# Kernel tuning notes

Hardware: AMD Instinct MI355X
Metric: run time of the kernel (lower is better)

## Reference

```python
import jax, jax.numpy as jnp
import numpy as np

T, G, K, N = 8192, 8, 1024, 2048

def setup_inputs() -> dict:
    key = jax.random.key(0)
    k1, k2, k3 = jax.random.split(key, 3)
    x = jax.random.normal(k1, (T, K), dtype=jnp.float32)
    w = jax.random.normal(k2, (G, N, K), dtype=jnp.float32) * 0.02
    # cumulative end-offsets per group: sorted, last entry == T (covers all tokens)
    offs = jnp.sort(jax.random.randint(k3, (G,), 0, T).astype(jnp.int32))
    offs = offs.at[-1].set(T)
    return {"input": x, "weight": w, "grouped_mm_offs": offs}

def reference(input, weight, grouped_mm_offs):
    # grouped_mm(input, weight.transpose(1,2), offs): token t in group g iff
    # offs[g-1] <= t < offs[g]; out[t] = input[t] @ weight[g].T
    t = input.shape[0]
    g = weight.shape[0]
    gid = jnp.searchsorted(grouped_mm_offs, jnp.arange(t), side="right")  # [T]
    out = jnp.zeros((t, weight.shape[1]), dtype=input.dtype)
    for gi in range(g):  # fixed small expert loop; data dims stay vectorized
        xg = jnp.where((gid == gi)[:, None], input, jnp.zeros((), input.dtype))
        out = out + xg @ weight[gi].T
    return out
```

## Files before the change

### kernel.cpp

```cpp
#include <hip/hip_runtime.h>
#include <hip/hip_bf16.h>


#define T_DIM 8192
#define G_DIM 8
#define K_DIM 1024
#define N_DIM 2048
#define MAX_PAIRS 72

using short8  = __attribute__((ext_vector_type(8))) short;
using f32x4   = __attribute__((ext_vector_type(4))) float;
using ushort8 = __attribute__((ext_vector_type(8))) unsigned short;

typedef __attribute__((address_space(1))) void gvoid;
typedef __attribute__((address_space(3))) void lvoid;

__global__ __launch_bounds__(256) void cvt_kernel(const float* __restrict__ x,
                                                  const float* __restrict__ w,
                                                  ushort8* __restrict__ xb,
                                                  ushort8* __restrict__ wb,
                                                  int n8x, int n8tot) {
  const int stride = gridDim.x * blockDim.x;
  for (int i = blockIdx.x * blockDim.x + threadIdx.x; i < n8tot; i += 2 * stride) {
#pragma unroll
    for (int u = 0; u < 2; ++u) {
      const int idx = i + u * stride;
      if (idx >= n8tot) break;
      const f32x4* s; ushort8* d; int j;
      if (idx < n8x) { s = (const f32x4*)x; d = xb; j = idx; }
      else           { s = (const f32x4*)w; d = wb; j = idx - n8x; }
      f32x4 v0 = __builtin_nontemporal_load(&s[2 * j]);
      f32x4 v1 = __builtin_nontemporal_load(&s[2 * j + 1]);
      ushort8 o;
      o[0] = __builtin_bit_cast(unsigned short, __float2bfloat16(v0[0]));
      o[1] = __builtin_bit_cast(unsigned short, __float2bfloat16(v0[1]));
      o[2] = __builtin_bit_cast(unsigned short, __float2bfloat16(v0[2]));
      o[3] = __builtin_bit_cast(unsigned short, __float2bfloat16(v0[3]));
      o[4] = __builtin_bit_cast(unsigned short, __float2bfloat16(v1[0]));
      o[5] = __builtin_bit_cast(unsigned short, __float2bfloat16(v1[1]));
      o[6] = __builtin_bit_cast(unsigned short, __float2bfloat16(v1[2]));
      o[7] = __builtin_bit_cast(unsigned short, __float2bfloat16(v1[3]));
      d[j] = o;
    }
  }
}

__global__ __launch_bounds__(256, 4) void grouped_gemm_kernel(
    const __hip_bfloat16* __restrict__ xb,
    const __hip_bfloat16* __restrict__ wb,
    const int* __restrict__ offs,
    float* __restrict__ out) {
  int offv[G_DIM];
#pragma unroll
  for (int i = 0; i < G_DIM; ++i) offv[i] = offs[i];

  const int p = blockIdx.y;
  int g = -1, tile = 0, lo = 0, hi = 0, pre = 0;
#pragma unroll
  for (int gi = 0; gi < G_DIM; ++gi) {
    const int l = gi ? offv[gi - 1] : 0;
    const int h = offv[gi];
    const int t0 = l >> 7;
    const int cnt = (h > l) ? (((h + 127) >> 7) - t0) : 0;
    if (g < 0 && p < pre + cnt) { g = gi; tile = t0 + (p - pre); lo = l; hi = h; }
    pre += cnt;
  }
  if (g < 0) return;

  const int m0 = tile * 128;
  const int n0 = blockIdx.x * 128;

  __shared__ __align__(16) __hip_bfloat16 As[128 * 64];
  __shared__ __align__(16) __hip_bfloat16 Bs[128 * 64];

  const __hip_bfloat16* wg = wb + (size_t)g * N_DIM * K_DIM;

  const int lane = threadIdx.x & 63;
  const int wid  = threadIdx.x >> 6;
  const int wm   = wid >> 1;
  const int wn   = wid & 1;

  const int srow = lane >> 3;
  const int scol = ((lane & 7) ^ srow) * 8;

  f32x4 acc[4][4] = {};

  for (int kk = 0; kk < K_DIM / 64; ++kk) {
    const int k0 = kk * 64;
#pragma unroll
    for (int i = 0; i < 4; ++i) {
      const int j   = wid * 4 + i;
      const int row = j * 8 + srow;
      const __hip_bfloat16* ga = xb + (size_t)(m0 + row) * K_DIM + k0 + scol;
      const __hip_bfloat16* gb = wg + (size_t)(n0 + row) * K_DIM + k0 + scol;
      __builtin_amdgcn_global_load_lds((gvoid*)ga, (lvoid*)(As + j * 512), 16, 0, 0);
      __builtin_amdgcn_global_load_lds((gvoid*)gb, (lvoid*)(Bs + j * 512), 16, 0, 0);
    }
    __syncthreads();

#pragma unroll
    for (int ks = 0; ks < 2; ++ks) {
      const int kb  = ks * 4 + (lane >> 4);
      const int off = ((kb ^ (lane & 7)) * 8);
      short8 a[4], b[4];
#pragma unroll
      for (int mt = 0; mt < 4; ++mt)
        a[mt] = *reinterpret_cast<const short8*>(
            As + (wm * 64 + mt * 16 + (lane & 15)) * 64 + off);
#pragma unroll
      for (int nt = 0; nt < 4; ++nt)
        b[nt] = *reinterpret_cast<const short8*>(
            Bs + (wn * 64 + nt * 16 + (lane & 15)) * 64 + off);
#pragma unroll
      for (int mt = 0; mt < 4; ++mt)
#pragma unroll
        for (int nt = 0; nt < 4; ++nt)
          acc[mt][nt] = __builtin_amdgcn_mfma_f32_16x16x32_bf16(
              a[mt], b[nt], acc[mt][nt], 0, 0, 0);
    }
    __syncthreads();
  }

  const int quad = lane >> 4;
#pragma unroll
  for (int mt = 0; mt < 4; ++mt) {
    const int rbase = m0 + wm * 64 + mt * 16 + quad * 4;
#pragma unroll
    for (int r = 0; r < 4; ++r) {
      const int row = rbase + r;
      if (row < lo || row >= hi) continue;
#pragma unroll
      for (int nt = 0; nt < 4; ++nt) {
        const int col = n0 + wn * 64 + nt * 16 + (lane & 15);
        out[(size_t)row * N_DIM + col] = acc[mt][nt][r];
      }
    }
  }
}

__global__ __launch_bounds__(256) void fallback_kernel(
    const float* __restrict__ x, const float* __restrict__ w,
    const int* __restrict__ offs, float* __restrict__ out) {
  __shared__ float xs[K_DIM];
  const int t = blockIdx.y;
  int g = 0;
  while (g < G_DIM - 1 && offs[g] <= t) ++g;
  for (int i = threadIdx.x; i < K_DIM; i += blockDim.x)
    xs[i] = x[(size_t)t * K_DIM + i];
  __syncthreads();
  const int n = blockIdx.x * blockDim.x + threadIdx.x;
  const float* wr = w + ((size_t)g * N_DIM + n) * K_DIM;
  float s = 0.f;
  for (int k = 0; k < K_DIM; ++k) s += xs[k] * wr[k];
  out[(size_t)t * N_DIM + n] = s;
}

extern "C" void kernel_launch(void* const* d_in, const int* in_sizes, int n_in,
                              void* d_out, int out_size, void* d_ws, size_t ws_size,
                              hipStream_t stream) {
  const float* x    = (const float*)d_in[0];
  const float* w    = (const float*)d_in[1];
  const int*   offs = (const int*)d_in[2];
  float*       out  = (float*)d_out;

  const size_t x_elems = (size_t)T_DIM * K_DIM;
  const size_t w_elems = (size_t)G_DIM * N_DIM * K_DIM;
  const size_t need    = (x_elems + w_elems) * sizeof(__hip_bfloat16);

  if (ws_size < need) {
    fallback_kernel<<<dim3(N_DIM / 256, T_DIM), 256, 0, stream>>>(x, w, offs, out);
    return;
  }

  __hip_bfloat16* xb = (__hip_bfloat16*)d_ws;
  __hip_bfloat16* wb = xb + x_elems;

  const int n8x   = (int)(x_elems / 8);
  const int n8tot = (int)((x_elems + w_elems) / 8);
  cvt_kernel<<<4096, 256, 0, stream>>>(x, w, (ushort8*)xb, (ushort8*)wb,
                                       n8x, n8tot);

  grouped_gemm_kernel<<<dim3(N_DIM / 128, MAX_PAIRS), 256, 0, stream>>>(
      xb, wb, offs, out);
}
```

Baseline: 183.9 us.

## Triple-buffer LDS loads, widen tile to 128x256 with 512 threads, remap blocks

```diff
diff --git a/kernel.cpp b/kernel.cpp
--- a/kernel.cpp
+++ b/kernel.cpp
@@ -7,6 +7,8 @@
 #define K_DIM 1024
 #define N_DIM 2048
 #define MAX_PAIRS 72
+#define PPX (MAX_PAIRS / 8)
+#define NT (K_DIM / 64)
 
 using short8  = __attribute__((ext_vector_type(8))) short;
 using f32x4   = __attribute__((ext_vector_type(4))) float;
@@ -45,16 +47,20 @@
   }
 }
 
-__global__ __launch_bounds__(256, 4) void grouped_gemm_kernel(
+__global__ __launch_bounds__(512) void grouped_gemm_kernel(
     const __hip_bfloat16* __restrict__ xb,
     const __hip_bfloat16* __restrict__ wb,
     const int* __restrict__ offs,
     float* __restrict__ out) {
+  const int v  = blockIdx.y * 8 + blockIdx.x;
+  const int p  = (v & 7) * PPX + ((v >> 3) % PPX);
+  const int nb = (v >> 3) / PPX;
+  const int n0 = nb * 256;
+
   int offv[G_DIM];
 #pragma unroll
   for (int i = 0; i < G_DIM; ++i) offv[i] = offs[i];
 
-  const int p = blockIdx.y;
   int g = -1, tile = 0, lo = 0, hi = 0, pre = 0;
 #pragma unroll
   for (int gi = 0; gi < G_DIM; ++gi) {
@@ -68,58 +74,94 @@
   if (g < 0) return;
 
   const int m0 = tile * 128;
-  const int n0 = blockIdx.x * 128;
-
-  __shared__ __align__(16) __hip_bfloat16 As[128 * 64];
-  __shared__ __align__(16) __hip_bfloat16 Bs[128 * 64];
+
+  __shared__ __align__(16) __hip_bfloat16 As[3 * 128 * 64];
+  __shared__ __align__(16) __hip_bfloat16 Bs[3 * 256 * 64];
 
   const __hip_bfloat16* wg = wb + (size_t)g * N_DIM * K_DIM;
 
   const int lane = threadIdx.x & 63;
   const int wid  = threadIdx.x >> 6;
-  const int wm   = wid >> 1;
-  const int wn   = wid & 1;
+  const int wm   = wid >> 2;
+  const int wn   = wid & 3;
 
   const int srow = lane >> 3;
   const int scol = ((lane & 7) ^ srow) * 8;
 
+  const __hip_bfloat16* gA0 = xb + (size_t)(m0 + (wid * 2 + 0) * 8 + srow) * K_DIM + scol;
+  const __hip_bfloat16* gA1 = xb + (size_t)(m0 + (wid * 2 + 1) * 8 + srow) * K_DIM + scol;
+  const __hip_bfloat16* gB0 = wg + (size_t)(n0 + (wid * 4 + 0) * 8 + srow) * K_DIM + scol;
+  const __hip_bfloat16* gB1 = wg + (size_t)(n0 + (wid * 4 + 1) * 8 + srow) * K_DIM + scol;
+  const __hip_bfloat16* gB2 = wg + (size_t)(n0 + (wid * 4 + 2) * 8 + srow) * K_DIM + scol;
+  const __hip_bfloat16* gB3 = wg + (size_t)(n0 + (wid * 4 + 3) * 8 + srow) * K_DIM + scol;
+
+  __hip_bfloat16* Ad = As + (wid * 2) * 512 + lane * 8;
+  __hip_bfloat16* Bd = Bs + (wid * 4) * 512 + lane * 8;
+
+  auto stage = [&](int tt, int bb) {
+    const int ko = tt * 64;
+    __hip_bfloat16* Adb = Ad + bb * (128 * 64);
+    __hip_bfloat16* Bdb = Bd + bb * (256 * 64);
+    __builtin_amdgcn_global_load_lds((gvoid*)(gA0 + ko), (lvoid*)(Adb),        16, 0, 0);
+    __builtin_amdgcn_global_load_lds((gvoid*)(gA1 + ko), (lvoid*)(Adb + 512),  16, 0, 0);
+    __builtin_amdgcn_global_load_lds((gvoid*)(gB0 + ko), (lvoid*)(Bdb),        16, 0, 0);
+    __builtin_amdgcn_global_load_lds((gvoid*)(gB1 + ko), (lvoid*)(Bdb + 512),  16, 0, 0);
+    __builtin_amdgcn_global_load_lds((gvoid*)(gB2 + ko), (lvoid*)(Bdb + 1024), 16, 0, 0);
+    __builtin_amdgcn_global_load_lds((gvoid*)(gB3 + ko), (lvoid*)(Bdb + 1536), 16, 0, 0);
+  };
+
   f32x4 acc[4][4] = {};
 
-  for (int kk = 0; kk < K_DIM / 64; ++kk) {
-    const int k0 = kk * 64;
-#pragma unroll
-    for (int i = 0; i < 4; ++i) {
-      const int j   = wid * 4 + i;
-      const int row = j * 8 + srow;
-      const __hip_bfloat16* ga = xb + (size_t)(m0 + row) * K_DIM + k0 + scol;
-      const __hip_bfloat16* gb = wg + (size_t)(n0 + row) * K_DIM + k0 + scol;
-      __builtin_amdgcn_global_load_lds((gvoid*)ga, (lvoid*)(As + j * 512), 16, 0, 0);
-      __builtin_amdgcn_global_load_lds((gvoid*)gb, (lvoid*)(Bs + j * 512), 16, 0, 0);
-    }
-    __syncthreads();
-
+  auto compute_tile = [&](int bb) {
+    const __hip_bfloat16* Ab = As + bb * (128 * 64);
+    const __hip_bfloat16* Bb = Bs + bb * (256 * 64);
+    short8 a[2][4], b[2][4];
 #pragma unroll
     for (int ks = 0; ks < 2; ++ks) {
       const int kb  = ks * 4 + (lane >> 4);
-      const int off = ((kb ^ (lane & 7)) * 8);
-      short8 a[4], b[4];
+      const int off = (kb ^ (lane & 7)) * 8;
 #pragma unroll
       for (int mt = 0; mt < 4; ++mt)
-        a[mt] = *reinterpret_cast<const short8*>(
-            As + (wm * 64 + mt * 16 + (lane & 15)) * 64 + off);
+        a[ks][mt] = *reinterpret_cast<const short8*>(
+            Ab + (wm * 64 + mt * 16 + (lane & 15)) * 64 + off);
 #pragma unroll
       for (int nt = 0; nt < 4; ++nt)
-        b[nt] = *reinterpret_cast<const short8*>(
-            Bs + (wn * 64 + nt * 16 + (lane & 15)) * 64 + off);
+        b[ks][nt] = *reinterpret_cast<const short8*>(
+            Bb + (wn * 64 + nt * 16 + (lane & 15)) * 64 + off);
+    }
+    __builtin_amdgcn_s_setprio(1);
+#pragma unroll
+    for (int ks = 0; ks < 2; ++ks)
 #pragma unroll
       for (int mt = 0; mt < 4; ++mt)
 #pragma unroll
         for (int nt = 0; nt < 4; ++nt)
           acc[mt][nt] = __builtin_amdgcn_mfma_f32_16x16x32_bf16(
-              a[mt], b[nt], acc[mt][nt], 0, 0, 0);
-    }
-    __syncthreads();
-  }
+              a[ks][mt], b[ks][nt], acc[mt][nt], 0, 0, 0);
+    __builtin_amdgcn_s_setprio(0);
+  };
+
+  stage(0, 0);
+  stage(1, 1);
+
+  for (int t = 0; t < NT - 2; ++t) {
+    const int buf = t % 3;
+    stage(t + 2, (t + 2) % 3);
+    asm volatile("s_waitcnt vmcnt(12)" ::: "memory");
+    __builtin_amdgcn_s_barrier();
+    asm volatile("" ::: "memory");
+    compute_tile(buf);
+    asm volatile("" ::: "memory");
+    __builtin_amdgcn_s_barrier();
+  }
+  asm volatile("s_waitcnt vmcnt(6)" ::: "memory");
+  __builtin_amdgcn_s_barrier();
+  asm volatile("" ::: "memory");
+  compute_tile((NT - 2) % 3);
+  asm volatile("s_waitcnt vmcnt(0)" ::: "memory");
+  __builtin_amdgcn_s_barrier();
+  asm volatile("" ::: "memory");
+  compute_tile((NT - 1) % 3);
 
   const int quad = lane >> 4;
 #pragma unroll
@@ -180,6 +222,6 @@
   cvt_kernel<<<4096, 256, 0, stream>>>(x, w, (ushort8*)xb, (ushort8*)wb,
                                        n8x, n8tot);
 
-  grouped_gemm_kernel<<<dim3(N_DIM / 128, MAX_PAIRS), 256, 0, stream>>>(
+  grouped_gemm_kernel<<<dim3(N_DIM / 256, MAX_PAIRS), 512, 0, stream>>>(
       xb, wb, offs, out);
 }
```

New measurement: 206.1 us. 1.12x slower.

## Fuse weight fp32-to-bf16 conversion into GEMM with register-prefetched B tiles

Applied to the files above, without the earlier changes.

```diff
diff --git a/kernel.cpp b/kernel.cpp
--- a/kernel.cpp
+++ b/kernel.cpp
@@ -7,6 +7,7 @@
 #define K_DIM 1024
 #define N_DIM 2048
 #define MAX_PAIRS 72
+#define NT (K_DIM / 64)
 
 using short8  = __attribute__((ext_vector_type(8))) short;
 using f32x4   = __attribute__((ext_vector_type(4))) float;
@@ -15,65 +16,58 @@
 typedef __attribute__((address_space(1))) void gvoid;
 typedef __attribute__((address_space(3))) void lvoid;
 
-__global__ __launch_bounds__(256) void cvt_kernel(const float* __restrict__ x,
-                                                  const float* __restrict__ w,
-                                                  ushort8* __restrict__ xb,
-                                                  ushort8* __restrict__ wb,
-                                                  int n8x, int n8tot) {
+__global__ __launch_bounds__(256) void cvt_x_kernel(const float* __restrict__ x,
+                                                    ushort8* __restrict__ xb,
+                                                    int n8) {
   const int stride = gridDim.x * blockDim.x;
-  for (int i = blockIdx.x * blockDim.x + threadIdx.x; i < n8tot; i += 2 * stride) {
-#pragma unroll
-    for (int u = 0; u < 2; ++u) {
-      const int idx = i + u * stride;
-      if (idx >= n8tot) break;
-      const f32x4* s; ushort8* d; int j;
-      if (idx < n8x) { s = (const f32x4*)x; d = xb; j = idx; }
-      else           { s = (const f32x4*)w; d = wb; j = idx - n8x; }
-      f32x4 v0 = __builtin_nontemporal_load(&s[2 * j]);
-      f32x4 v1 = __builtin_nontemporal_load(&s[2 * j + 1]);
-      ushort8 o;
-      o[0] = __builtin_bit_cast(unsigned short, __float2bfloat16(v0[0]));
-      o[1] = __builtin_bit_cast(unsigned short, __float2bfloat16(v0[1]));
-      o[2] = __builtin_bit_cast(unsigned short, __float2bfloat16(v0[2]));
-      o[3] = __builtin_bit_cast(unsigned short, __float2bfloat16(v0[3]));
-      o[4] = __builtin_bit_cast(unsigned short, __float2bfloat16(v1[0]));
-      o[5] = __builtin_bit_cast(unsigned short, __float2bfloat16(v1[1]));
-      o[6] = __builtin_bit_cast(unsigned short, __float2bfloat16(v1[2]));
-      o[7] = __builtin_bit_cast(unsigned short, __float2bfloat16(v1[3]));
-      d[j] = o;
-    }
+  for (int i = blockIdx.x * blockDim.x + threadIdx.x; i < n8; i += stride) {
+    f32x4 v0 = __builtin_nontemporal_load(&((const f32x4*)x)[2 * i]);
+    f32x4 v1 = __builtin_nontemporal_load(&((const f32x4*)x)[2 * i + 1]);
+    ushort8 o;
+    o[0] = __builtin_bit_cast(unsigned short, __float2bfloat16(v0[0]));
+    o[1] = __builtin_bit_cast(unsigned short, __float2bfloat16(v0[1]));
+    o[2] = __builtin_bit_cast(unsigned short, __float2bfloat16(v0[2]));
+    o[3] = __builtin_bit_cast(unsigned short, __float2bfloat16(v0[3]));
+    o[4] = __builtin_bit_cast(unsigned short, __float2bfloat16(v1[0]));
+    o[5] = __builtin_bit_cast(unsigned short, __float2bfloat16(v1[1]));
+    o[6] = __builtin_bit_cast(unsigned short, __float2bfloat16(v1[2]));
+    o[7] = __builtin_bit_cast(unsigned short, __float2bfloat16(v1[3]));
+    xb[i] = o;
   }
 }
 
 __global__ __launch_bounds__(256, 4) void grouped_gemm_kernel(
     const __hip_bfloat16* __restrict__ xb,
-    const __hip_bfloat16* __restrict__ wb,
+    const float* __restrict__ w,
     const int* __restrict__ offs,
     float* __restrict__ out) {
+  const int v  = blockIdx.y * 16 + blockIdx.x;
+  const int c  = v & 7;
+  const int l  = v >> 3;
+  const int nb = c * 2 + (l & 1);
+  const int p  = l >> 1;
+  const int n0 = nb * 128;
+
   int offv[G_DIM];
 #pragma unroll
   for (int i = 0; i < G_DIM; ++i) offv[i] = offs[i];
 
-  const int p = blockIdx.y;
   int g = -1, tile = 0, lo = 0, hi = 0, pre = 0;
 #pragma unroll
   for (int gi = 0; gi < G_DIM; ++gi) {
-    const int l = gi ? offv[gi - 1] : 0;
-    const int h = offv[gi];
-    const int t0 = l >> 7;
-    const int cnt = (h > l) ? (((h + 127) >> 7) - t0) : 0;
-    if (g < 0 && p < pre + cnt) { g = gi; tile = t0 + (p - pre); lo = l; hi = h; }
+    const int lb = gi ? offv[gi - 1] : 0;
+    const int hb = offv[gi];
+    const int t0 = lb >> 7;
+    const int cnt = (hb > lb) ? (((hb + 127) >> 7) - t0) : 0;
+    if (g < 0 && p < pre + cnt) { g = gi; tile = t0 + (p - pre); lo = lb; hi = hb; }
     pre += cnt;
   }
   if (g < 0) return;
 
   const int m0 = tile * 128;
-  const int n0 = blockIdx.x * 128;
 
   __shared__ __align__(16) __hip_bfloat16 As[128 * 64];
   __shared__ __align__(16) __hip_bfloat16 Bs[128 * 64];
-
-  const __hip_bfloat16* wg = wb + (size_t)g * N_DIM * K_DIM;
 
   const int lane = threadIdx.x & 63;
   const int wid  = threadIdx.x >> 6;
@@ -82,21 +76,62 @@
 
   const int srow = lane >> 3;
   const int scol = ((lane & 7) ^ srow) * 8;
+  const int lcol = (lane & 7) * 8;
+
+  const __hip_bfloat16* gA[4];
+  const float*          gB[4];
+  __hip_bfloat16*       Bd[4];
+#pragma unroll
+  for (int i = 0; i < 4; ++i) {
+    const int j   = wid * 4 + i;
+    const int row = j * 8 + srow;
+    gA[i] = xb + (size_t)(m0 + row) * K_DIM + scol;
+    gB[i] = w + ((size_t)g * N_DIM + n0 + row) * K_DIM + lcol;
+    Bd[i] = Bs + j * 512 + srow * 64 + scol;
+  }
+
+  f32x4 breg[4][2];
 
   f32x4 acc[4][4] = {};
 
-  for (int kk = 0; kk < K_DIM / 64; ++kk) {
+#pragma unroll
+  for (int i = 0; i < 4; ++i) {
+    breg[i][0] = *(const f32x4*)(gB[i]);
+    breg[i][1] = *(const f32x4*)(gB[i] + 4);
+  }
+
+  for (int kk = 0; kk < NT; ++kk) {
     const int k0 = kk * 64;
 #pragma unroll
+    for (int i = 0; i < 4; ++i)
+      __builtin_amdgcn_global_load_lds((gvoid*)(gA[i] + k0),
+                                       (lvoid*)(As + (wid * 4 + i) * 512), 16, 0, 0);
+    asm volatile("s_waitcnt vmcnt(4)" ::: "memory");
+#pragma unroll
     for (int i = 0; i < 4; ++i) {
-      const int j   = wid * 4 + i;
-      const int row = j * 8 + srow;
-      const __hip_bfloat16* ga = xb + (size_t)(m0 + row) * K_DIM + k0 + scol;
-      const __hip_bfloat16* gb = wg + (size_t)(n0 + row) * K_DIM + k0 + scol;
-      __builtin_amdgcn_global_load_lds((gvoid*)ga, (lvoid*)(As + j * 512), 16, 0, 0);
-      __builtin_amdgcn_global_load_lds((gvoid*)gb, (lvoid*)(Bs + j * 512), 16, 0, 0);
-    }
-    __syncthreads();
+      ushort8 o;
+      o[0] = __builtin_bit_cast(unsigned short, __float2bfloat16(breg[i][0][0]));
+      o[1] = __builtin_bit_cast(unsigned short, __float2bfloat16(breg[i][0][1]));
+      o[2] = __builtin_bit_cast(unsigned short, __float2bfloat16(breg[i][0][2]));
+      o[3] = __builtin_bit_cast(unsigned short, __float2bfloat16(breg[i][0][3]));
+      o[4] = __builtin_bit_cast(unsigned short, __float2bfloat16(breg[i][1][0]));
+      o[5] = __builtin_bit_cast(unsigned short, __float2bfloat16(breg[i][1][1]));
+      o[6] = __builtin_bit_cast(unsigned short, __float2bfloat16(breg[i][1][2]));
+      o[7] = __builtin_bit_cast(unsigned short, __float2bfloat16(breg[i][1][3]));
+      *(ushort8*)(Bd[i]) = o;
+    }
+    if (kk + 1 < NT) {
+#pragma unroll
+      for (int i = 0; i < 4; ++i) {
+        breg[i][0] = *(const f32x4*)(gB[i] + k0 + 64);
+        breg[i][1] = *(const f32x4*)(gB[i] + k0 + 64 + 4);
+      }
+      asm volatile("s_waitcnt vmcnt(8) lgkmcnt(0)" ::: "memory");
+    } else {
+      asm volatile("s_waitcnt vmcnt(0) lgkmcnt(0)" ::: "memory");
+    }
+    __builtin_amdgcn_s_barrier();
+    asm volatile("" ::: "memory");
 
 #pragma unroll
     for (int ks = 0; ks < 2; ++ks) {
@@ -118,7 +153,8 @@
           acc[mt][nt] = __builtin_amdgcn_mfma_f32_16x16x32_bf16(
               a[mt], b[nt], acc[mt][nt], 0, 0, 0);
     }
-    __syncthreads();
+    asm volatile("" ::: "memory");
+    __builtin_amdgcn_s_barrier();
   }
 
   const int quad = lane >> 4;
@@ -164,8 +200,7 @@
   float*       out  = (float*)d_out;
 
   const size_t x_elems = (size_t)T_DIM * K_DIM;
-  const size_t w_elems = (size_t)G_DIM * N_DIM * K_DIM;
-  const size_t need    = (x_elems + w_elems) * sizeof(__hip_bfloat16);
+  const size_t need    = x_elems * sizeof(__hip_bfloat16);
 
   if (ws_size < need) {
     fallback_kernel<<<dim3(N_DIM / 256, T_DIM), 256, 0, stream>>>(x, w, offs, out);
@@ -173,13 +208,9 @@
   }
 
   __hip_bfloat16* xb = (__hip_bfloat16*)d_ws;
-  __hip_bfloat16* wb = xb + x_elems;
-
-  const int n8x   = (int)(x_elems / 8);
-  const int n8tot = (int)((x_elems + w_elems) / 8);
-  cvt_kernel<<<4096, 256, 0, stream>>>(x, w, (ushort8*)xb, (ushort8*)wb,
-                                       n8x, n8tot);
-
-  grouped_gemm_kernel<<<dim3(N_DIM / 128, MAX_PAIRS), 256, 0, stream>>>(
-      xb, wb, offs, out);
-}
+  const int n8 = (int)(x_elems / 8);
+
+  cvt_x_kernel<<<2048, 256, 0, stream>>>(x, (ushort8*)xb, n8);
+
+  grouped_gemm_kernel<<<dim3(16, MAX_PAIRS), 256, 0, stream>>>(xb, w, offs, out);
+}
```

Measured after the change: 233.7 us. +27.1%, slower.

## Use 128x256 tiles with 8 waves and remap block order for weight reuse

Applied to the files above, without the earlier changes.

```diff
diff --git a/kernel.cpp b/kernel.cpp
--- a/kernel.cpp
+++ b/kernel.cpp
@@ -7,6 +7,8 @@
 #define K_DIM 1024
 #define N_DIM 2048
 #define MAX_PAIRS 72
+#define PPX (MAX_PAIRS / 8)
+#define NT (K_DIM / 64)
 
 using short8  = __attribute__((ext_vector_type(8))) short;
 using f32x4   = __attribute__((ext_vector_type(4))) float;
@@ -45,16 +47,20 @@
   }
 }
 
-__global__ __launch_bounds__(256, 4) void grouped_gemm_kernel(
+__global__ __launch_bounds__(512, 4) void grouped_gemm_kernel(
     const __hip_bfloat16* __restrict__ xb,
     const __hip_bfloat16* __restrict__ wb,
     const int* __restrict__ offs,
     float* __restrict__ out) {
+  const int v  = blockIdx.y * 8 + blockIdx.x;
+  const int p  = (v & 7) * PPX + ((v >> 3) % PPX);
+  const int nb = (v >> 3) / PPX;
+  const int n0 = nb * 256;
+
   int offv[G_DIM];
 #pragma unroll
   for (int i = 0; i < G_DIM; ++i) offv[i] = offs[i];
 
-  const int p = blockIdx.y;
   int g = -1, tile = 0, lo = 0, hi = 0, pre = 0;
 #pragma unroll
   for (int gi = 0; gi < G_DIM; ++gi) {
@@ -68,34 +74,45 @@
   if (g < 0) return;
 
   const int m0 = tile * 128;
-  const int n0 = blockIdx.x * 128;
 
   __shared__ __align__(16) __hip_bfloat16 As[128 * 64];
-  __shared__ __align__(16) __hip_bfloat16 Bs[128 * 64];
+  __shared__ __align__(16) __hip_bfloat16 Bs[256 * 64];
 
   const __hip_bfloat16* wg = wb + (size_t)g * N_DIM * K_DIM;
 
   const int lane = threadIdx.x & 63;
   const int wid  = threadIdx.x >> 6;
-  const int wm   = wid >> 1;
-  const int wn   = wid & 1;
+  const int wm   = wid >> 2;
+  const int wn   = wid & 3;
 
   const int srow = lane >> 3;
   const int scol = ((lane & 7) ^ srow) * 8;
 
+  const __hip_bfloat16* gA[2];
+  const __hip_bfloat16* gB[4];
+#pragma unroll
+  for (int i = 0; i < 2; ++i) {
+    const int j = wid * 2 + i;
+    gA[i] = xb + (size_t)(m0 + j * 8 + srow) * K_DIM + scol;
+  }
+#pragma unroll
+  for (int i = 0; i < 4; ++i) {
+    const int j = wid * 4 + i;
+    gB[i] = wg + (size_t)(n0 + j * 8 + srow) * K_DIM + scol;
+  }
+
   f32x4 acc[4][4] = {};
 
-  for (int kk = 0; kk < K_DIM / 64; ++kk) {
+  for (int kk = 0; kk < NT; ++kk) {
     const int k0 = kk * 64;
 #pragma unroll
-    for (int i = 0; i < 4; ++i) {
-      const int j   = wid * 4 + i;
-      const int row = j * 8 + srow;
-      const __hip_bfloat16* ga = xb + (size_t)(m0 + row) * K_DIM + k0 + scol;
-      const __hip_bfloat16* gb = wg + (size_t)(n0 + row) * K_DIM + k0 + scol;
-      __builtin_amdgcn_global_load_lds((gvoid*)ga, (lvoid*)(As + j * 512), 16, 0, 0);
-      __builtin_amdgcn_global_load_lds((gvoid*)gb, (lvoid*)(Bs + j * 512), 16, 0, 0);
-    }
+    for (int i = 0; i < 2; ++i)
+      __builtin_amdgcn_global_load_lds((gvoid*)(gA[i] + k0),
+                                       (lvoid*)(As + (wid * 2 + i) * 512), 16, 0, 0);
+#pragma unroll
+    for (int i = 0; i < 4; ++i)
+      __builtin_amdgcn_global_load_lds((gvoid*)(gB[i] + k0),
+                                       (lvoid*)(Bs + (wid * 4 + i) * 512), 16, 0, 0);
     __syncthreads();
 
 #pragma unroll
@@ -180,6 +197,6 @@
   cvt_kernel<<<4096, 256, 0, stream>>>(x, w, (ushort8*)xb, (ushort8*)wb,
                                        n8x, n8tot);
 
-  grouped_gemm_kernel<<<dim3(N_DIM / 128, MAX_PAIRS), 256, 0, stream>>>(
+  grouped_gemm_kernel<<<dim3(8, MAX_PAIRS), 512, 0, stream>>>(
       xb, wb, offs, out);
 }
```

After: 194.4 us. 5.7% more time.
